# Kernel tuning notes

Hardware: AMD Instinct MI355X
Metric: run time of the kernel (lower is better)

## Reference

```python
import jax, jax.numpy as jnp
import numpy as np
from jax import lax

K = 16               # kNN neighbors
SAMPLING_RATIO = 0.25
BN_EPS = 1e-5


def farthest_point_sample(p, M):
    """Iterative FPS. p: (B,N,3) -> (B,M) int32 indices. Starts at index 0 (as pointnet2_ops)."""
    B, N, _ = p.shape
    batch = jnp.arange(B)

    def step(carry, _):
        dist, last = carry                       # dist: (B,N) min sq-dist to selected set
        sel = p[batch, last]                     # (B,3) last selected point
        d = jnp.sum((p - sel[:, None, :]) ** 2, axis=-1)  # (B,N)
        dist = jnp.minimum(dist, d)
        nxt = jnp.argmax(dist, axis=-1).astype(jnp.int32)
        return (dist, nxt), nxt

    first = jnp.zeros((B,), jnp.int32)
    init_dist = jnp.full((B, N), 1e10, jnp.float32)
    (_, _), rest = lax.scan(step, (init_dist, first), None, length=M - 1)  # rest: (M-1,B)
    return jnp.concatenate([first[None, :], rest], axis=0).T  # (B,M)


def knn(p2, p1, k):
    """For each query in p2:(B,M,3) find k nearest in p1:(B,N,3). Returns (B,M,k) indices."""
    # squared distances via ||a||^2 + ||b||^2 - 2 a.b  -> (B,M,N)
    d = (jnp.sum(p2 * p2, -1)[:, :, None]
         + jnp.sum(p1 * p1, -1)[:, None, :]
         - 2.0 * jnp.einsum('bmd,bnd->bmn', p2, p1))
    _, idx = lax.top_k(-d, k)
    return idx


def setup_inputs() -> dict:
    key = jax.random.key(0)
    k1, k2, k3 = jax.random.split(key, 3)
    B, N, Cin, Cout = 8, 8192, 64, 128
    x = jax.random.normal(k1, (B, N, Cin), jnp.float32)
    p1 = jax.random.normal(k2, (B, N, 3), jnp.float32)
    W = jax.random.normal(k3, (Cout, Cin), jnp.float32) * 0.1  # Conv1d k=1, no bias
    gamma = jnp.ones((Cout,), jnp.float32)   # BatchNorm weight
    beta = jnp.zeros((Cout,), jnp.float32)   # BatchNorm bias
    return {"x": x, "p1": p1, "W": W, "gamma": gamma, "beta": beta}


def reference(x, p1, W, gamma, beta):
    B, N, Cin = x.shape
    M = int(N * SAMPLING_RATIO)

    fps_idx = farthest_point_sample(p1, M)                         # (B,M)
    p2 = jnp.take_along_axis(p1, fps_idx[:, :, None], axis=1)      # (B,M,3)
    neighbors = knn(p2, p1, K)                                     # (B,M,K)

    # pointwise conv (1x1) + BatchNorm1d (train-mode batch stats over B*N) + ReLU
    h = jnp.einsum('bnc,oc->bno', x, W)                            # (B,N,Cout)
    mean = jnp.mean(h, axis=(0, 1))
    var = jnp.var(h, axis=(0, 1))
    h = gamma * (h - mean) * lax.rsqrt(var + BN_EPS) + beta
    h = jax.nn.relu(h)

    Cout = h.shape[-1]
    feats = jnp.take_along_axis(h, neighbors.reshape(B, M * K, 1), axis=1)
    feats = feats.reshape(B, M, K, Cout)                           # index_points gather
    y = jnp.max(feats, axis=2)                                     # max-pool over k neighbors
    return y, p2
```

## Files before the change

### kernel.cpp

```cpp
#include <hip/hip_runtime.h>
#include <cstdint>

#define B_   8
#define N_   8192
#define M_   2048
#define CIN  64
#define COUT 128

typedef unsigned long long u64;

__device__ __forceinline__ float sq3(float dx, float dy, float dz) {
    return __fadd_rn(__fadd_rn(__fmul_rn(dx, dx), __fmul_rn(dy, dy)), __fmul_rn(dz, dz));
}

template<int CTRL>
__device__ __forceinline__ double dppmax(double x) {
    long long b = __double_as_longlong(x);
    int lo = (int)b, hi = (int)(b >> 32);
    int plo = __builtin_amdgcn_update_dpp(lo, lo, CTRL, 0xf, 0xf, false);
    int phi = __builtin_amdgcn_update_dpp(hi, hi, CTRL, 0xf, 0xf, false);
    double p = __longlong_as_double(((long long)(unsigned)phi << 32) | (unsigned)plo);
    return fmax(x, p);
}

__global__ __launch_bounds__(512) void phase1_kernel(const float* __restrict__ p1, float* __restrict__ p2,
                                                     const float* __restrict__ x, const float* __restrict__ W,
                                                     float* __restrict__ h) {
    __shared__ __align__(16) char smem[98432];
    int t = threadIdx.x;

    if (blockIdx.x < B_) {
        float2* lds_xy = (float2*)smem;
        float*  lds_z  = (float*)(smem + 65536);
        double* wbest  = (double*)(smem + 98304);

        int b = blockIdx.x;
        const float* pb = p1 + (size_t)b * N_ * 3;
        float* p2b = p2 + (size_t)b * M_ * 3;
        int lane = t & 63, wave = t >> 6;

        for (int i = t; i < N_; i += 512) {
            lds_xy[i] = make_float2(pb[3 * i], pb[3 * i + 1]);
            lds_z[i]  = pb[3 * i + 2];
        }
        __syncthreads();

        float px[16], py[16], pz[16], dist[16];
#pragma unroll
        for (int j = 0; j < 16; ++j) {
            int idx = t + j * 512;
            float2 xy = lds_xy[idx];
            px[j] = xy.x; py[j] = xy.y; pz[j] = lds_z[idx];
            dist[j] = 1e10f;
        }

        float2 s0 = lds_xy[0];
        float sx = s0.x, sy = s0.y, sz = lds_z[0];

        for (int i = 1; i < M_; ++i) {
            if (t == ((i & 7) << 6)) {
                p2b[3 * (i - 1)] = sx; p2b[3 * (i - 1) + 1] = sy; p2b[3 * (i - 1) + 2] = sz;
            }
            float bestv = -1.0f; int besti = 0;
#pragma unroll
            for (int j = 0; j < 16; ++j) {
                float d = sq3(__fsub_rn(px[j], sx), __fsub_rn(py[j], sy), __fsub_rn(pz[j], sz));
                float nd = fminf(dist[j], d);
                dist[j] = nd;
                if (nd > bestv) { bestv = nd; besti = t + j * 512; }
            }
            double key = __longlong_as_double(__double_as_longlong((double)bestv) | (u64)(8191 - besti));
            key = dppmax<0x121>(key);
            key = dppmax<0x122>(key);
            key = dppmax<0x124>(key);
            key = dppmax<0x128>(key);
            key = dppmax<0x142>(key);
            key = dppmax<0x143>(key);
            int buf = (i & 1) << 3;
            if (lane == 63) wbest[buf + wave] = key;
            __syncthreads();
            double2 k01 = *(double2*)&wbest[buf];
            double2 k23 = *(double2*)&wbest[buf + 2];
            double2 k45 = *(double2*)&wbest[buf + 4];
            double2 k67 = *(double2*)&wbest[buf + 6];
            double km = fmax(fmax(fmax(k01.x, k01.y), fmax(k23.x, k23.y)),
                             fmax(fmax(k45.x, k45.y), fmax(k67.x, k67.y)));
            int w = 8191 - (int)(__double_as_longlong(km) & 0x1fff);
            float2 sxy = lds_xy[w];
            sx = sxy.x; sy = sxy.y; sz = lds_z[w];
        }
        if (t == 0) {
            p2b[3 * (M_ - 1)] = sx; p2b[3 * (M_ - 1) + 1] = sy; p2b[3 * (M_ - 1) + 2] = sz;
        }
    } else {
        float (*xs)[65] = (float (*)[65])smem;
        float (*ws)[65] = (float (*)[65])(smem + 33280);
        size_t rowBase = (size_t)(blockIdx.x - B_) * 128;
        for (int idx = t; idx < COUT * CIN; idx += 512) ws[idx >> 6][idx & 63] = W[idx];
        const float* xb = x + rowBase * CIN;
        for (int idx = t; idx < 128 * CIN; idx += 512) xs[idx >> 6][idx & 63] = xb[idx];
        __syncthreads();
        int r0 = (t & 31) * 4, c0 = (t >> 5) * 8;
        float acc[4][8];
#pragma unroll
        for (int i = 0; i < 4; ++i)
#pragma unroll
            for (int j = 0; j < 8; ++j) acc[i][j] = 0.f;
        for (int k = 0; k < CIN; ++k) {
            float xv[4], wvv[8];
#pragma unroll
            for (int i = 0; i < 4; ++i) xv[i] = xs[r0 + i][k];
#pragma unroll
            for (int j = 0; j < 8; ++j) wvv[j] = ws[c0 + j][k];
#pragma unroll
            for (int i = 0; i < 4; ++i)
#pragma unroll
                for (int j = 0; j < 8; ++j) acc[i][j] = fmaf(xv[i], wvv[j], acc[i][j]);
        }
#pragma unroll
        for (int i = 0; i < 4; ++i) {
            size_t o = (rowBase + r0 + i) * COUT + c0;
            *(float4*)&h[o]     = make_float4(acc[i][0], acc[i][1], acc[i][2], acc[i][3]);
            *(float4*)&h[o + 4] = make_float4(acc[i][4], acc[i][5], acc[i][6], acc[i][7]);
        }
    }
}

__global__ __launch_bounds__(256) void bn_partial(const float* __restrict__ h, float* __restrict__ psum,
                                                  float* __restrict__ psq) {
    int t = threadIdx.x;
    int c = t & 127, half = t >> 7;
    size_t base = (size_t)blockIdx.x * 256;
    float s = 0.f, q = 0.f;
    for (int it = 0; it < 128; ++it) {
        float v = h[(base + it * 2 + half) * COUT + c];
        s += v; q = fmaf(v, v, q);
    }
    __shared__ float ls[256], lq[256];
    ls[t] = s; lq[t] = q;
    __syncthreads();
    if (t < 128) {
        psum[blockIdx.x * 128 + c] = ls[t] + ls[t + 128];
        psq[blockIdx.x * 128 + c]  = lq[t] + lq[t + 128];
    }
}

__global__ void bn_final(const float* __restrict__ psum, const float* __restrict__ psq,
                         const float* __restrict__ gamma, const float* __restrict__ beta,
                         float* __restrict__ bns) {
    int c = threadIdx.x;
    float s = 0.f, q = 0.f;
    for (int i = 0; i < 256; ++i) { s += psum[i * 128 + c]; q += psq[i * 128 + c]; }
    float mean = s / 65536.0f;
    float var  = q / 65536.0f - mean * mean;
    float sc = gamma[c] * rsqrtf(var + 1e-5f);
    bns[c] = sc;
    bns[128 + c] = beta[c] - mean * sc;
}

__global__ __launch_bounds__(256) void knn_kernel(const float* __restrict__ p1, const float* __restrict__ p2,
                                                  const float* __restrict__ h, const float* __restrict__ bns,
                                                  float* __restrict__ y) {
    int q = blockIdx.x * 4 + (threadIdx.x >> 6);
    int lane = threadIdx.x & 63;
    int b = q >> 11;
    const float* pb = p1 + (size_t)b * N_ * 3;
    const float* pq = p2 + (size_t)q * 3;
    float qx = pq[0], qy = pq[1], qz = pq[2];
    float sqq = __fadd_rn(__fadd_rn(__fmul_rn(qx, qx), __fmul_rn(qy, qy)), __fmul_rn(qz, qz));

    float ld = 1e30f; int li = 0;
    float tau = 1e30f;

    for (int c0 = 0; c0 < N_; c0 += 64) {
        int cand = c0 + lane;
        float ax = pb[3 * cand], ay = pb[3 * cand + 1], az = pb[3 * cand + 2];
        float s1 = __fadd_rn(__fadd_rn(__fmul_rn(ax, ax), __fmul_rn(ay, ay)), __fmul_rn(az, az));
        float dt = __fadd_rn(__fadd_rn(__fmul_rn(ax, qx), __fmul_rn(ay, qy)), __fmul_rn(az, qz));
        float d  = __fsub_rn(__fadd_rn(sqq, s1), __fmul_rn(2.0f, dt));
        unsigned long long mk = __ballot(d < tau);
        while (mk) {
            int l = __ffsll((unsigned long long)mk) - 1;
            mk &= mk - 1;
            float dd = __shfl(d, l);
            int   ii = c0 + l;
            int pos = __popcll(__ballot(ld <= dd) & 0xFFFFull);
            if (pos < 16) {
                float pd = __shfl_up(ld, 1);
                int   pi = __shfl_up(li, 1);
                if (lane < 16) {
                    if (lane > pos) { ld = pd; li = pi; }
                    if (lane == pos) { ld = dd; li = ii; }
                }
                tau = __shfl(ld, 15);
            }
        }
    }

    int c = lane << 1;
    float sc0 = bns[c], sc1 = bns[c + 1];
    float sh0 = bns[128 + c], sh1 = bns[128 + c + 1];
    float a0 = -1e30f, a1 = -1e30f;
#pragma unroll
    for (int t16 = 0; t16 < 16; ++t16) {
        int nb = __shfl(li, t16);
        const float* hp = h + (((size_t)(b * N_ + nb)) << 7) + c;
        float h0 = hp[0], h1 = hp[1];
        a0 = fmaxf(a0, fmaf(h0, sc0, sh0));
        a1 = fmaxf(a1, fmaf(h1, sc1, sh1));
    }
    float2 out = make_float2(fmaxf(a0, 0.f), fmaxf(a1, 0.f));
    *(float2*)&y[((size_t)q << 7) + c] = out;
}

extern "C" void kernel_launch(void* const* d_in, const int* in_sizes, int n_in,
                              void* d_out, int out_size, void* d_ws, size_t ws_size,
                              hipStream_t stream) {
    const float* x     = (const float*)d_in[0];
    const float* p1    = (const float*)d_in[1];
    const float* W     = (const float*)d_in[2];
    const float* gamma = (const float*)d_in[3];
    const float* beta  = (const float*)d_in[4];

    float* y  = (float*)d_out;
    float* p2 = y + (size_t)B_ * M_ * COUT;

    float* h    = (float*)d_ws;
    float* psum = h + (size_t)B_ * N_ * COUT;
    float* psq  = psum + 256 * 128;
    float* bns  = psq + 256 * 128;

    phase1_kernel<<<B_ + (B_ * N_) / 128, 512, 0, stream>>>(p1, p2, x, W, h);
    bn_partial<<<256, 256, 0, stream>>>(h, psum, psq);
    bn_final<<<1, 128, 0, stream>>>(psum, psq, gamma, beta, bns);
    knn_kernel<<<(B_ * M_) / 4, 256, 0, stream>>>(p1, p2, h, bns, y);
}
```

Baseline: 2.084 ms.

## Pack two FPS batches per 1024-thread block and read points from global memory

The FPS stage now runs two batch elements per 1024-thread block (4 blocks instead of 8), with each 512-thread half reducing independently. The LDS point cache is removed: the selected point is re-read from global memory (likely L1/L2 cached) every iteration. The GEMM blocks also move to 1024 threads with a 4x4 register tile. The cost is that both halves now share one __syncthreads per iteration, and each iteration adds a global load on the serial critical path.

```diff
diff --git a/kernel.cpp b/kernel.cpp
--- a/kernel.cpp
+++ b/kernel.cpp
@@ -6,6 +6,7 @@
 #define M_   2048
 #define CIN  64
 #define COUT 128
+#define FPSBLK 4
 
 typedef unsigned long long u64;
 
@@ -23,42 +24,33 @@
     return fmax(x, p);
 }
 
-__global__ __launch_bounds__(512) void phase1_kernel(const float* __restrict__ p1, float* __restrict__ p2,
-                                                     const float* __restrict__ x, const float* __restrict__ W,
-                                                     float* __restrict__ h) {
-    __shared__ __align__(16) char smem[98432];
+__global__ __launch_bounds__(1024) void phase1_kernel(const float* __restrict__ p1, float* __restrict__ p2,
+                                                      const float* __restrict__ x, const float* __restrict__ W,
+                                                      float* __restrict__ h) {
+    __shared__ __align__(16) char smem[66560];
     int t = threadIdx.x;
 
-    if (blockIdx.x < B_) {
-        float2* lds_xy = (float2*)smem;
-        float*  lds_z  = (float*)(smem + 65536);
-        double* wbest  = (double*)(smem + 98304);
-
-        int b = blockIdx.x;
+    if (blockIdx.x < FPSBLK) {
+        double* wbest = (double*)smem;
+        int wave = t >> 6, lane = t & 63;
+        int sub = wave >> 3, wv = wave & 7;
+        int tl = t & 511;
+        int b = blockIdx.x * 2 + sub;
         const float* pb = p1 + (size_t)b * N_ * 3;
         float* p2b = p2 + (size_t)b * M_ * 3;
-        int lane = t & 63, wave = t >> 6;
-
-        for (int i = t; i < N_; i += 512) {
-            lds_xy[i] = make_float2(pb[3 * i], pb[3 * i + 1]);
-            lds_z[i]  = pb[3 * i + 2];
-        }
-        __syncthreads();
 
         float px[16], py[16], pz[16], dist[16];
 #pragma unroll
         for (int j = 0; j < 16; ++j) {
-            int idx = t + j * 512;
-            float2 xy = lds_xy[idx];
-            px[j] = xy.x; py[j] = xy.y; pz[j] = lds_z[idx];
+            int idx = tl + j * 512;
+            px[j] = pb[3 * idx]; py[j] = pb[3 * idx + 1]; pz[j] = pb[3 * idx + 2];
             dist[j] = 1e10f;
         }
 
-        float2 s0 = lds_xy[0];
-        float sx = s0.x, sy = s0.y, sz = lds_z[0];
+        float sx = pb[0], sy = pb[1], sz = pb[2];
 
         for (int i = 1; i < M_; ++i) {
-            if (t == ((i & 7) << 6)) {
+            if (wv == (i & 7) && lane == 0) {
                 p2b[3 * (i - 1)] = sx; p2b[3 * (i - 1) + 1] = sy; p2b[3 * (i - 1) + 2] = sz;
             }
             float bestv = -1.0f; int besti = 0;
@@ -67,7 +59,7 @@
                 float d = sq3(__fsub_rn(px[j], sx), __fsub_rn(py[j], sy), __fsub_rn(pz[j], sz));
                 float nd = fminf(dist[j], d);
                 dist[j] = nd;
-                if (nd > bestv) { bestv = nd; besti = t + j * 512; }
+                if (nd > bestv) { bestv = nd; besti = tl + j * 512; }
             }
             double key = __longlong_as_double(__double_as_longlong((double)bestv) | (u64)(8191 - besti));
             key = dppmax<0x121>(key);
@@ -76,52 +68,50 @@
             key = dppmax<0x128>(key);
             key = dppmax<0x142>(key);
             key = dppmax<0x143>(key);
-            int buf = (i & 1) << 3;
-            if (lane == 63) wbest[buf + wave] = key;
+            int base = ((i & 1) << 4) + (sub << 3);
+            if (lane == 63) wbest[base + wv] = key;
             __syncthreads();
-            double2 k01 = *(double2*)&wbest[buf];
-            double2 k23 = *(double2*)&wbest[buf + 2];
-            double2 k45 = *(double2*)&wbest[buf + 4];
-            double2 k67 = *(double2*)&wbest[buf + 6];
+            double2 k01 = *(double2*)&wbest[base];
+            double2 k23 = *(double2*)&wbest[base + 2];
+            double2 k45 = *(double2*)&wbest[base + 4];
+            double2 k67 = *(double2*)&wbest[base + 6];
             double km = fmax(fmax(fmax(k01.x, k01.y), fmax(k23.x, k23.y)),
                              fmax(fmax(k45.x, k45.y), fmax(k67.x, k67.y)));
             int w = 8191 - (int)(__double_as_longlong(km) & 0x1fff);
-            float2 sxy = lds_xy[w];
-            sx = sxy.x; sy = sxy.y; sz = lds_z[w];
-        }
-        if (t == 0) {
+            sx = pb[3 * w]; sy = pb[3 * w + 1]; sz = pb[3 * w + 2];
+        }
+        if (tl == 0) {
             p2b[3 * (M_ - 1)] = sx; p2b[3 * (M_ - 1) + 1] = sy; p2b[3 * (M_ - 1) + 2] = sz;
         }
     } else {
         float (*xs)[65] = (float (*)[65])smem;
         float (*ws)[65] = (float (*)[65])(smem + 33280);
-        size_t rowBase = (size_t)(blockIdx.x - B_) * 128;
-        for (int idx = t; idx < COUT * CIN; idx += 512) ws[idx >> 6][idx & 63] = W[idx];
+        size_t rowBase = (size_t)(blockIdx.x - FPSBLK) * 128;
+        for (int idx = t; idx < COUT * CIN; idx += 1024) ws[idx >> 6][idx & 63] = W[idx];
         const float* xb = x + rowBase * CIN;
-        for (int idx = t; idx < 128 * CIN; idx += 512) xs[idx >> 6][idx & 63] = xb[idx];
+        for (int idx = t; idx < 128 * CIN; idx += 1024) xs[idx >> 6][idx & 63] = xb[idx];
         __syncthreads();
-        int r0 = (t & 31) * 4, c0 = (t >> 5) * 8;
-        float acc[4][8];
+        int r0 = (t & 31) * 4, c0 = (t >> 5) * 4;
+        float acc[4][4];
 #pragma unroll
         for (int i = 0; i < 4; ++i)
 #pragma unroll
-            for (int j = 0; j < 8; ++j) acc[i][j] = 0.f;
+            for (int j = 0; j < 4; ++j) acc[i][j] = 0.f;
         for (int k = 0; k < CIN; ++k) {
-            float xv[4], wvv[8];
+            float xv[4], wvv[4];
 #pragma unroll
             for (int i = 0; i < 4; ++i) xv[i] = xs[r0 + i][k];
 #pragma unroll
-            for (int j = 0; j < 8; ++j) wvv[j] = ws[c0 + j][k];
+            for (int j = 0; j < 4; ++j) wvv[j] = ws[c0 + j][k];
 #pragma unroll
             for (int i = 0; i < 4; ++i)
 #pragma unroll
-                for (int j = 0; j < 8; ++j) acc[i][j] = fmaf(xv[i], wvv[j], acc[i][j]);
+                for (int j = 0; j < 4; ++j) acc[i][j] = fmaf(xv[i], wvv[j], acc[i][j]);
         }
 #pragma unroll
         for (int i = 0; i < 4; ++i) {
             size_t o = (rowBase + r0 + i) * COUT + c0;
-            *(float4*)&h[o]     = make_float4(acc[i][0], acc[i][1], acc[i][2], acc[i][3]);
-            *(float4*)&h[o + 4] = make_float4(acc[i][4], acc[i][5], acc[i][6], acc[i][7]);
+            *(float4*)&h[o] = make_float4(acc[i][0], acc[i][1], acc[i][2], acc[i][3]);
         }
     }
 }
@@ -230,7 +220,7 @@
     float* psq  = psum + 256 * 128;
     float* bns  = psq + 256 * 128;
 
-    phase1_kernel<<<B_ + (B_ * N_) / 128, 512, 0, stream>>>(p1, p2, x, W, h);
+    phase1_kernel<<<FPSBLK + (B_ * N_) / 128, 1024, 0, stream>>>(p1, p2, x, W, h);
     bn_partial<<<256, 256, 0, stream>>>(h, psum, psq);
     bn_final<<<1, 128, 0, stream>>>(psum, psq, gamma, beta, bns);
     knn_kernel<<<(B_ * M_) / 4, 256, 0, stream>>>(p1, p2, h, bns, y);
```

Result: slower. 3.599 ms (+72.7%).

## Process two FPS batches per block and read point coordinates from global memory

Applied to the files above, without the earlier changes.

The farthest-point-sampling stage now assigns two batch elements to each block, using 4 blocks instead of 8, and interleaves their distance updates and DPP max reductions. The per-iteration barrier and reduction latency is shared between two independent chains. To make room in registers for two distance arrays, point coordinates are no longer cached in registers or LDS. They are re-read from global memory every iteration, with a strided 3-float layout, and the selected point is also fetched from global. This adds a lot of cache traffic and latency on the serial FPS critical path, and that may outweigh the gain from overlapping the two chains.

```diff
diff --git a/kernel.cpp b/kernel.cpp
--- a/kernel.cpp
+++ b/kernel.cpp
@@ -6,6 +6,7 @@
 #define M_   2048
 #define CIN  64
 #define COUT 128
+#define FPSBLK 4
 
 typedef unsigned long long u64;
 
@@ -26,76 +27,80 @@
 __global__ __launch_bounds__(512) void phase1_kernel(const float* __restrict__ p1, float* __restrict__ p2,
                                                      const float* __restrict__ x, const float* __restrict__ W,
                                                      float* __restrict__ h) {
-    __shared__ __align__(16) char smem[98432];
+    __shared__ __align__(16) char smem[66560];
     int t = threadIdx.x;
 
-    if (blockIdx.x < B_) {
-        float2* lds_xy = (float2*)smem;
-        float*  lds_z  = (float*)(smem + 65536);
-        double* wbest  = (double*)(smem + 98304);
-
-        int b = blockIdx.x;
-        const float* pb = p1 + (size_t)b * N_ * 3;
-        float* p2b = p2 + (size_t)b * M_ * 3;
-        int lane = t & 63, wave = t >> 6;
-
-        for (int i = t; i < N_; i += 512) {
-            lds_xy[i] = make_float2(pb[3 * i], pb[3 * i + 1]);
-            lds_z[i]  = pb[3 * i + 2];
-        }
-        __syncthreads();
-
-        float px[16], py[16], pz[16], dist[16];
-#pragma unroll
-        for (int j = 0; j < 16; ++j) {
-            int idx = t + j * 512;
-            float2 xy = lds_xy[idx];
-            px[j] = xy.x; py[j] = xy.y; pz[j] = lds_z[idx];
-            dist[j] = 1e10f;
-        }
-
-        float2 s0 = lds_xy[0];
-        float sx = s0.x, sy = s0.y, sz = lds_z[0];
+    if (blockIdx.x < FPSBLK) {
+        double* wbest = (double*)smem;
+        int lane = t & 63, wv = t >> 6;
+        int b0 = blockIdx.x * 2, b1 = b0 + 1;
+        const float* pA = p1 + (size_t)b0 * N_ * 3;
+        const float* pB = p1 + (size_t)b1 * N_ * 3;
+        float* p2A = p2 + (size_t)b0 * M_ * 3;
+        float* p2B = p2 + (size_t)b1 * M_ * 3;
+
+        float distA[16], distB[16];
+#pragma unroll
+        for (int j = 0; j < 16; ++j) { distA[j] = 1e10f; distB[j] = 1e10f; }
+
+        float sxA = pA[0], syA = pA[1], szA = pA[2];
+        float sxB = pB[0], syB = pB[1], szB = pB[2];
 
         for (int i = 1; i < M_; ++i) {
-            if (t == ((i & 7) << 6)) {
-                p2b[3 * (i - 1)] = sx; p2b[3 * (i - 1) + 1] = sy; p2b[3 * (i - 1) + 2] = sz;
+            if (wv == (i & 7)) {
+                if (lane == 0)  { p2A[3*(i-1)] = sxA; p2A[3*(i-1)+1] = syA; p2A[3*(i-1)+2] = szA; }
+                if (lane == 32) { p2B[3*(i-1)] = sxB; p2B[3*(i-1)+1] = syB; p2B[3*(i-1)+2] = szB; }
             }
-            float bestv = -1.0f; int besti = 0;
+            float bvA = -1.0f; int biA = 0;
+            float bvB = -1.0f; int biB = 0;
 #pragma unroll
             for (int j = 0; j < 16; ++j) {
-                float d = sq3(__fsub_rn(px[j], sx), __fsub_rn(py[j], sy), __fsub_rn(pz[j], sz));
-                float nd = fminf(dist[j], d);
-                dist[j] = nd;
-                if (nd > bestv) { bestv = nd; besti = t + j * 512; }
+                int idx = t + j * 512;
+                const float* qa = pA + 3 * idx;
+                const float* qb = pB + 3 * idx;
+                float ax = qa[0], ay = qa[1], az = qa[2];
+                float bx = qb[0], by = qb[1], bz = qb[2];
+                float dA = sq3(__fsub_rn(ax, sxA), __fsub_rn(ay, syA), __fsub_rn(az, szA));
+                float dB = sq3(__fsub_rn(bx, sxB), __fsub_rn(by, syB), __fsub_rn(bz, szB));
+                float ndA = fminf(distA[j], dA);
+                float ndB = fminf(distB[j], dB);
+                distA[j] = ndA;
+                distB[j] = ndB;
+                if (ndA > bvA) { bvA = ndA; biA = idx; }
+                if (ndB > bvB) { bvB = ndB; biB = idx; }
             }
-            double key = __longlong_as_double(__double_as_longlong((double)bestv) | (u64)(8191 - besti));
-            key = dppmax<0x121>(key);
-            key = dppmax<0x122>(key);
-            key = dppmax<0x124>(key);
-            key = dppmax<0x128>(key);
-            key = dppmax<0x142>(key);
-            key = dppmax<0x143>(key);
-            int buf = (i & 1) << 3;
-            if (lane == 63) wbest[buf + wave] = key;
+            double kA = __longlong_as_double(__double_as_longlong((double)bvA) | (u64)(8191 - biA));
+            double kB = __longlong_as_double(__double_as_longlong((double)bvB) | (u64)(8191 - biB));
+            kA = dppmax<0x121>(kA); kB = dppmax<0x121>(kB);
+            kA = dppmax<0x122>(kA); kB = dppmax<0x122>(kB);
+            kA = dppmax<0x124>(kA); kB = dppmax<0x124>(kB);
+            kA = dppmax<0x128>(kA); kB = dppmax<0x128>(kB);
+            kA = dppmax<0x142>(kA); kB = dppmax<0x142>(kB);
+            kA = dppmax<0x143>(kA); kB = dppmax<0x143>(kB);
+            int buf = (i & 1) << 4;
+            if (lane == 63) { wbest[buf + wv] = kA; wbest[buf + 8 + wv] = kB; }
             __syncthreads();
-            double2 k01 = *(double2*)&wbest[buf];
-            double2 k23 = *(double2*)&wbest[buf + 2];
-            double2 k45 = *(double2*)&wbest[buf + 4];
-            double2 k67 = *(double2*)&wbest[buf + 6];
-            double km = fmax(fmax(fmax(k01.x, k01.y), fmax(k23.x, k23.y)),
-                             fmax(fmax(k45.x, k45.y), fmax(k67.x, k67.y)));
-            int w = 8191 - (int)(__double_as_longlong(km) & 0x1fff);
-            float2 sxy = lds_xy[w];
-            sx = sxy.x; sy = sxy.y; sz = lds_z[w];
-        }
-        if (t == 0) {
-            p2b[3 * (M_ - 1)] = sx; p2b[3 * (M_ - 1) + 1] = sy; p2b[3 * (M_ - 1) + 2] = sz;
-        }
+            const double2* WA = (const double2*)&wbest[buf];
+            const double2* WB = (const double2*)&wbest[buf + 8];
+            double2 a0 = WA[0], a1 = WA[1], a2 = WA[2], a3 = WA[3];
+            double2 c0 = WB[0], c1 = WB[1], c2 = WB[2], c3 = WB[3];
+            double mA = fmax(fmax(fmax(a0.x, a0.y), fmax(a1.x, a1.y)),
+                             fmax(fmax(a2.x, a2.y), fmax(a3.x, a3.y)));
+            double mB = fmax(fmax(fmax(c0.x, c0.y), fmax(c1.x, c1.y)),
+                             fmax(fmax(c2.x, c2.y), fmax(c3.x, c3.y)));
+            int wA = 8191 - (int)(__double_as_longlong(mA) & 0x1fff);
+            int wB = 8191 - (int)(__double_as_longlong(mB) & 0x1fff);
+            const float* sa = pA + 3 * wA;
+            const float* sb = pB + 3 * wB;
+            sxA = sa[0]; syA = sa[1]; szA = sa[2];
+            sxB = sb[0]; syB = sb[1]; szB = sb[2];
+        }
+        if (t == 0) { p2A[3*(M_-1)] = sxA; p2A[3*(M_-1)+1] = syA; p2A[3*(M_-1)+2] = szA; }
+        if (t == 1) { p2B[3*(M_-1)] = sxB; p2B[3*(M_-1)+1] = syB; p2B[3*(M_-1)+2] = szB; }
     } else {
         float (*xs)[65] = (float (*)[65])smem;
         float (*ws)[65] = (float (*)[65])(smem + 33280);
-        size_t rowBase = (size_t)(blockIdx.x - B_) * 128;
+        size_t rowBase = (size_t)(blockIdx.x - FPSBLK) * 128;
         for (int idx = t; idx < COUT * CIN; idx += 512) ws[idx >> 6][idx & 63] = W[idx];
         const float* xb = x + rowBase * CIN;
         for (int idx = t; idx < 128 * CIN; idx += 512) xs[idx >> 6][idx & 63] = xb[idx];
@@ -230,7 +235,7 @@
     float* psq  = psum + 256 * 128;
     float* bns  = psq + 256 * 128;
 
-    phase1_kernel<<<B_ + (B_ * N_) / 128, 512, 0, stream>>>(p1, p2, x, W, h);
+    phase1_kernel<<<FPSBLK + (B_ * N_) / 128, 512, 0, stream>>>(p1, p2, x, W, h);
     bn_partial<<<256, 256, 0, stream>>>(h, psum, psq);
     bn_final<<<1, 128, 0, stream>>>(psum, psq, gamma, beta, bns);
     knn_kernel<<<(B_ * M_) / 4, 256, 0, stream>>>(p1, p2, h, bns, y);
```

Result: slower. 4.084 ms (+95.9%).
